# Kernel optimization log

Measured on AMD Instinct MI355X. Metric: run time of the kernel, lower is better.

## Reference

```python
import jax, jax.numpy as jnp
import numpy as np

TEMPERATURE = 0.07
EPS = 1e-12  # matches torch F.normalize default eps


def setup_inputs() -> dict:
    key = jax.random.key(0)
    k1, k2 = jax.random.split(key)
    features1 = jax.random.normal(k1, (16384, 512), dtype=jnp.float32)
    features2 = jax.random.normal(k2, (16384, 512), dtype=jnp.float32)
    return {"features1": features1, "features2": features2}


def _l2_normalize(x):
    # torch F.normalize: x / max(||x||, eps)
    norm = jnp.sqrt(jnp.sum(x * x, axis=1, keepdims=True))
    return x / jnp.maximum(norm, EPS)


def reference(features1, features2):
    f1 = _l2_normalize(features1)
    f2 = _l2_normalize(features2)
    # [N, N] similarity logits
    logits = jnp.einsum('nd,md->nm', f1, f2) / TEMPERATURE
    n = logits.shape[0]
    # cross-entropy with labels = arange(n): mean over rows of (logsumexp - diag logit)
    log_probs = jax.nn.log_softmax(logits, axis=1)
    diag = jnp.diagonal(log_probs)
    loss = -jnp.mean(diag)
    return loss
```

## Files before the change

### kernel.cpp

```cpp
#include <hip/hip_runtime.h>
#include <stdint.h>

#define NROWS 16384
#define KDIM  512
#define BM 128
#define BN 128
#define CT 4
#define NCHUNK 32
#define NPH 16
#define SLOT 16384
#define INV_T 14.285714285714286f
#define LOG2E 1.4426950408889634f

typedef __bf16 bf16x8 __attribute__((ext_vector_type(8)));
typedef float  f32x16 __attribute__((ext_vector_type(16)));
typedef unsigned short u16x8 __attribute__((ext_vector_type(8)));

__device__ __forceinline__ void gload_lds16(const void* gptr, void* lptr) {
    uint32_t loff = (uint32_t)(uintptr_t)lptr;
    loff = __builtin_amdgcn_readfirstlane(loff);
    __builtin_amdgcn_global_load_lds(
        (const uint32_t __attribute__((address_space(1)))*)(uintptr_t)gptr,
        (uint32_t __attribute__((address_space(3)))*)(uintptr_t)loff,
        16, 0, 0);
}


__global__ void k_norm(const float* __restrict__ X, char* __restrict__ Y, float scale) {
    const int row  = blockIdx.x * 4 + (threadIdx.x >> 6);
    const int lane = threadIdx.x & 63;
    const float* xr = X + (size_t)row * KDIM + lane * 8;
    float4 a = *(const float4*)xr;
    float4 b = *(const float4*)(xr + 4);
    float ss = a.x*a.x + a.y*a.y + a.z*a.z + a.w*a.w
             + b.x*b.x + b.y*b.y + b.z*b.z + b.w*b.w;
    #pragma unroll
    for (int off = 1; off < 64; off <<= 1) ss += __shfl_xor(ss, off);
    const float s = scale / fmaxf(sqrtf(ss), 1e-12f);
    __bf16 o[8];
    o[0] = (__bf16)(a.x * s); o[1] = (__bf16)(a.y * s);
    o[2] = (__bf16)(a.z * s); o[3] = (__bf16)(a.w * s);
    o[4] = (__bf16)(b.x * s); o[5] = (__bf16)(b.y * s);
    o[6] = (__bf16)(b.z * s); o[7] = (__bf16)(b.w * s);
    const int kh = lane >> 2, q = lane & 3;
    const size_t gr = ((size_t)(kh * 512 + (row >> 5)) * 2 + (q >> 1)) * 64
                    + ((q & 1) << 5) + (row & 31);
    *(u16x8*)(Y + gr * 16) = *(const u16x8*)o;
}

__global__ __launch_bounds__(256, 2) void k_gemm(const char* __restrict__ A,
                                                 const char* __restrict__ B,
                                                 float* __restrict__ S_part) {
    __shared__ __align__(16) char L[3 * SLOT];
    __shared__ float rowsum[2][BM];
    char* Lc = (char*)L;

    const int tid  = threadIdx.x;
    const int lane = tid & 63;
    const int w    = tid >> 6;
    const int wr   = w >> 1, wc = w & 1;
    const int bid  = blockIdx.x;
    const int xcd  = bid & 7;
    const int idx  = bid >> 3;
    const int st   = idx >> 5;
    const int wsub = idx & 31;
    const int sg   = xcd * 16 + st;
    const int bg   = sg & 15, cg = sg >> 4;
    const int brow  = (bg * 8 + (wsub >> 2)) * BM;
    const int chunk = cg * 4 + (wsub & 3);
    const int rbA0 = brow >> 5;

#define STGA(KH_, S_) do {                                                    \
        const char* g_ = A + ((size_t)((KH_) * 512 + rbA0) * 2048) + tid * 16;\
        char* l_ = Lc + (S_) * SLOT + tid * 16;                               \
        gload_lds16(g_,        l_);                                           \
        gload_lds16(g_ + 4096, l_ + 4096);                                    \
    } while (0)

#define STGB(KH_, S_) do {                                                    \
        const char* g_ = B + ((size_t)((KH_) * 512 + rbB0) * 2048) + tid * 16;\
        char* l_ = Lc + (S_) * SLOT + 8192 + tid * 16;                        \
        gload_lds16(g_,        l_);                                           \
        gload_lds16(g_ + 4096, l_ + 4096);                                    \
    } while (0)

#define RDS(HH_) do {                                                         \
        const char* sl_ = Lc + ((HH_) % 3) * SLOT;                            \
        _Pragma("unroll") for (int m_ = 0; m_ < 2; ++m_)                      \
        _Pragma("unroll") for (int ks_ = 0; ks_ < 2; ++ks_)                   \
            af[m_][ks_] = *(const bf16x8*)(sl_ + ((wr * 2 + m_) << 11)        \
                                           + (ks_ << 10) + (lane << 4));      \
        _Pragma("unroll") for (int n_ = 0; n_ < 2; ++n_)                      \
        _Pragma("unroll") for (int ks_ = 0; ks_ < 2; ++ks_)                   \
            bf[n_][ks_] = *(const bf16x8*)(sl_ + 8192 + ((wc * 2 + n_) << 11) \
                                           + (ks_ << 10) + (lane << 4));      \
    } while (0)

#define MM() do {                                                             \
        __builtin_amdgcn_s_setprio(1);                                        \
        _Pragma("unroll") for (int m_ = 0; m_ < 2; ++m_)                      \
        _Pragma("unroll") for (int n_ = 0; n_ < 2; ++n_)                      \
        _Pragma("unroll") for (int ks_ = 0; ks_ < 2; ++ks_)                   \
            acc[m_][n_] = __builtin_amdgcn_mfma_f32_32x32x16_bf16(            \
                af[m_][ks_], bf[n_][ks_], acc[m_][n_], 0, 0, 0);              \
        __builtin_amdgcn_s_setprio(0);                                        \
    } while (0)

    float rowacc = 0.f;
    #pragma unroll 1
    for (int ct = 0; ct < CT; ++ct) {
        const int rbB0 = chunk * 16 + ct * 4;
        f32x16 acc[2][2] = {};
        bf16x8 af[2][2], bf[2][2];

        STGA(0, 0); STGB(0, 0);
        STGA(1, 1); STGB(1, 1);
        asm volatile("s_waitcnt vmcnt(4)" ::: "memory");
        __builtin_amdgcn_s_barrier();

        #pragma unroll
        for (int h = 0; h < NPH; ++h) {
            RDS(h);
            if (h < NPH - 2) { STGA(h + 2, (h + 2) % 3); STGB(h + 2, (h + 2) % 3); }
            MM();
            if (h < NPH - 2)       asm volatile("s_waitcnt vmcnt(4)" ::: "memory");
            else if (h == NPH - 2) asm volatile("s_waitcnt vmcnt(0)" ::: "memory");
            __builtin_amdgcn_s_barrier();
        }

        #pragma unroll
        for (int m = 0; m < 2; ++m) {
            float rs[16];
            #pragma unroll
            for (int r = 0; r < 16; ++r)
                rs[r] = __builtin_amdgcn_exp2f(acc[m][0][r])
                      + __builtin_amdgcn_exp2f(acc[m][1][r]);
            #pragma unroll
            for (int off = 16; off >= 1; off >>= 1)
                #pragma unroll
                for (int r = 0; r < 16; ++r)
                    rs[r] += __shfl_xor(rs[r], off);
            if ((lane & 31) == 0) {
                const int rb = wr * 64 + m * 32 + (lane >> 5) * 4;
                #pragma unroll
                for (int r = 0; r < 16; ++r)
                    rowsum[wc][rb + (r & 3) + 8 * (r >> 2)] = rs[r];
            }
        }
        __syncthreads();
        if (tid < BM) rowacc += rowsum[0][tid] + rowsum[1][tid];
        __syncthreads();
    }
#undef STGA
#undef STGB
#undef RDS
#undef MM
    if (tid < BM) S_part[(size_t)chunk * NROWS + brow + tid] = rowacc;
}

__global__ void k_diag(const float* __restrict__ X1, const float* __restrict__ X2,
                       float* __restrict__ diag) {
    const int row  = blockIdx.x * 4 + (threadIdx.x >> 6);
    const int lane = threadIdx.x & 63;
    const float* x1 = X1 + (size_t)row * KDIM + lane * 8;
    const float* x2 = X2 + (size_t)row * KDIM + lane * 8;
    float4 a0 = *(const float4*)x1, a1 = *(const float4*)(x1 + 4);
    float4 b0 = *(const float4*)x2, b1 = *(const float4*)(x2 + 4);
    float s1 = a0.x*a0.x + a0.y*a0.y + a0.z*a0.z + a0.w*a0.w
             + a1.x*a1.x + a1.y*a1.y + a1.z*a1.z + a1.w*a1.w;
    float s2 = b0.x*b0.x + b0.y*b0.y + b0.z*b0.z + b0.w*b0.w
             + b1.x*b1.x + b1.y*b1.y + b1.z*b1.z + b1.w*b1.w;
    float dd = a0.x*b0.x + a0.y*b0.y + a0.z*b0.z + a0.w*b0.w
             + a1.x*b1.x + a1.y*b1.y + a1.z*b1.z + a1.w*b1.w;
    #pragma unroll
    for (int off = 1; off < 64; off <<= 1) {
        s1 += __shfl_xor(s1, off);
        s2 += __shfl_xor(s2, off);
        dd += __shfl_xor(dd, off);
    }
    if (lane == 0)
        diag[row] = dd / (fmaxf(sqrtf(s1), 1e-12f) * fmaxf(sqrtf(s2), 1e-12f)) * INV_T;
}

__global__ void k_loss(const float* __restrict__ S_part, const float* __restrict__ diag,
                       float* __restrict__ partial) {
    const int g = blockIdx.x * 256 + threadIdx.x;
    float S = 0.f;
    #pragma unroll
    for (int c = 0; c < NCHUNK; ++c) S += S_part[(size_t)c * NROWS + g];
    float v = logf(S) - diag[g];
    __shared__ float wsum[4];
    #pragma unroll
    for (int off = 1; off < 64; off <<= 1) v += __shfl_xor(v, off);
    if ((threadIdx.x & 63) == 0) wsum[threadIdx.x >> 6] = v;
    __syncthreads();
    if (threadIdx.x == 0) partial[blockIdx.x] = wsum[0] + wsum[1] + wsum[2] + wsum[3];
}

__global__ void k_final(const float* __restrict__ partial, float* __restrict__ out) {
    float v = partial[threadIdx.x];
    #pragma unroll
    for (int off = 1; off < 64; off <<= 1) v += __shfl_xor(v, off);
    if (threadIdx.x == 0) out[0] = v * (1.0f / (float)NROWS);
}

extern "C" void kernel_launch(void* const* d_in, const int* in_sizes, int n_in,
                              void* d_out, int out_size, void* d_ws, size_t ws_size,
                              hipStream_t stream) {
    const float* f1 = (const float*)d_in[0];
    const float* f2 = (const float*)d_in[1];
    float* out = (float*)d_out;

    char* ws = (char*)d_ws;
    char*  f1p   = ws;
    char*  f2p   = ws + (16u << 20);
    float* S_part = (float*)(ws + (32u << 20));
    float* diag   = (float*)(ws + (34u << 20));
    float* part   = (float*)(ws + (34u << 20) + (1u << 16));

    k_norm<<<dim3(NROWS / 4), dim3(256), 0, stream>>>(f1, f1p, INV_T * LOG2E);
    k_norm<<<dim3(NROWS / 4), dim3(256), 0, stream>>>(f2, f2p, 1.0f);
    k_gemm<<<dim3((NROWS / BM) * NCHUNK), dim3(256), 0, stream>>>(f1p, f2p, S_part);
    k_diag<<<dim3(NROWS / 4), dim3(256), 0, stream>>>(f1, f2, diag);
    k_loss<<<dim3(NROWS / 256), dim3(256), 0, stream>>>(S_part, diag, part);
    k_final<<<dim3(1), dim3(64), 0, stream>>>(part, out);
}
```

Measured before the change: 354.4 us.

## Use four-slot LDS ring and process two K-phases per barrier

The GEMM main loop moves from a three-slot LDS ring, with one K-phase and one barrier per step, to a four-slot ring. Each iteration now reads two K-phases into separate register fragment sets, stages the next two phases, and issues both sets of MFMAs before a single full vmcnt wait and barrier. The aim is to halve the barrier and waitcnt overhead and give the MFMAs larger batches. In exchange, shared memory per block grows to 64KB and fragment registers double. The full vmcnt(0) wait each iteration may also expose load latency that the old partial wait hid.

```diff
diff --git a/kernel.cpp b/kernel.cpp
--- a/kernel.cpp
+++ b/kernel.cpp
@@ -7,7 +7,7 @@
 #define BN 128
 #define CT 4
 #define NCHUNK 32
-#define NPH 16
+#define NIV 8
 #define SLOT 16384
 #define INV_T 14.285714285714286f
 #define LOG2E 1.4426950408889634f
@@ -51,7 +51,7 @@
 __global__ __launch_bounds__(256, 2) void k_gemm(const char* __restrict__ A,
                                                  const char* __restrict__ B,
                                                  float* __restrict__ S_part) {
-    __shared__ __align__(16) char L[3 * SLOT];
+    __shared__ __align__(16) char L[4 * SLOT];
     __shared__ float rowsum[2][BM];
     char* Lc = (char*)L;
 
@@ -84,25 +84,25 @@
         gload_lds16(g_ + 4096, l_ + 4096);                                    \
     } while (0)
 
-#define RDS(HH_) do {                                                         \
-        const char* sl_ = Lc + ((HH_) % 3) * SLOT;                            \
+#define RDS(SET_, HH_) do {                                                   \
+        const char* sl_ = Lc + ((HH_) & 3) * SLOT;                            \
         _Pragma("unroll") for (int m_ = 0; m_ < 2; ++m_)                      \
         _Pragma("unroll") for (int ks_ = 0; ks_ < 2; ++ks_)                   \
-            af[m_][ks_] = *(const bf16x8*)(sl_ + ((wr * 2 + m_) << 11)        \
+            af[SET_][m_][ks_] = *(const bf16x8*)(sl_ + ((wr * 2 + m_) << 11)  \
                                            + (ks_ << 10) + (lane << 4));      \
         _Pragma("unroll") for (int n_ = 0; n_ < 2; ++n_)                      \
         _Pragma("unroll") for (int ks_ = 0; ks_ < 2; ++ks_)                   \
-            bf[n_][ks_] = *(const bf16x8*)(sl_ + 8192 + ((wc * 2 + n_) << 11) \
-                                           + (ks_ << 10) + (lane << 4));      \
-    } while (0)
-
-#define MM() do {                                                             \
+            bf[SET_][n_][ks_] = *(const bf16x8*)(sl_ + 8192                   \
+                  + ((wc * 2 + n_) << 11) + (ks_ << 10) + (lane << 4));       \
+    } while (0)
+
+#define MM(SET_) do {                                                         \
         __builtin_amdgcn_s_setprio(1);                                        \
         _Pragma("unroll") for (int m_ = 0; m_ < 2; ++m_)                      \
         _Pragma("unroll") for (int n_ = 0; n_ < 2; ++n_)                      \
         _Pragma("unroll") for (int ks_ = 0; ks_ < 2; ++ks_)                   \
             acc[m_][n_] = __builtin_amdgcn_mfma_f32_32x32x16_bf16(            \
-                af[m_][ks_], bf[n_][ks_], acc[m_][n_], 0, 0, 0);              \
+                af[SET_][m_][ks_], bf[SET_][n_][ks_], acc[m_][n_], 0, 0, 0);  \
         __builtin_amdgcn_s_setprio(0);                                        \
     } while (0)
 
@@ -111,20 +111,26 @@
     for (int ct = 0; ct < CT; ++ct) {
         const int rbB0 = chunk * 16 + ct * 4;
         f32x16 acc[2][2] = {};
-        bf16x8 af[2][2], bf[2][2];
+        bf16x8 af[2][2][2], bf[2][2][2];
 
         STGA(0, 0); STGB(0, 0);
         STGA(1, 1); STGB(1, 1);
-        asm volatile("s_waitcnt vmcnt(4)" ::: "memory");
+        STGA(2, 2); STGB(2, 2);
+        STGA(3, 3); STGB(3, 3);
+        asm volatile("s_waitcnt vmcnt(8)" ::: "memory");
         __builtin_amdgcn_s_barrier();
 
         #pragma unroll
-        for (int h = 0; h < NPH; ++h) {
-            RDS(h);
-            if (h < NPH - 2) { STGA(h + 2, (h + 2) % 3); STGB(h + 2, (h + 2) % 3); }
-            MM();
-            if (h < NPH - 2)       asm volatile("s_waitcnt vmcnt(4)" ::: "memory");
-            else if (h == NPH - 2) asm volatile("s_waitcnt vmcnt(0)" ::: "memory");
+        for (int j = 0; j < NIV; ++j) {
+            RDS(0, 2 * j);
+            RDS(1, 2 * j + 1);
+            if (j >= 1 && j <= 6) {
+                STGA(2 * j + 2, (2 * j + 2) & 3); STGB(2 * j + 2, (2 * j + 2) & 3);
+                STGA(2 * j + 3, (2 * j + 3) & 3); STGB(2 * j + 3, (2 * j + 3) & 3);
+            }
+            MM(0);
+            MM(1);
+            asm volatile("s_waitcnt vmcnt(0)" ::: "memory");
             __builtin_amdgcn_s_barrier();
         }
 
```

After: 388.6 us. 9.6% more time.

## Load A fragments directly from global into double-buffered registers, stage only B via LDS

Applied to the files above, without the earlier changes.

The A operand of the similarity GEMM now bypasses shared memory. Each wave loads its A fragments straight from global memory into a register double buffer one k-phase ahead, and only B is staged through LDS with a three-slot ring. This halves LDS footprint and LDS read traffic and drops the explicit vmcnt waits inside the loop, relying instead on compiler-inserted waits for the register loads. In exchange, the two waves sharing A rows each fetch them from global or L2, which duplicates that traffic and raises register pressure. The correctness of the LDS staging now depends implicitly on in-order vmcnt completion.

```diff
diff --git a/kernel.cpp b/kernel.cpp
--- a/kernel.cpp
+++ b/kernel.cpp
@@ -8,7 +8,7 @@
 #define CT 4
 #define NCHUNK 32
 #define NPH 16
-#define SLOT 16384
+#define BSLOT 8192
 #define INV_T 14.285714285714286f
 #define LOG2E 1.4426950408889634f
 
@@ -51,7 +51,7 @@
 __global__ __launch_bounds__(256, 2) void k_gemm(const char* __restrict__ A,
                                                  const char* __restrict__ B,
                                                  float* __restrict__ S_part) {
-    __shared__ __align__(16) char L[3 * SLOT];
+    __shared__ __align__(16) char L[3 * BSLOT];
     __shared__ float rowsum[2][BM];
     char* Lc = (char*)L;
 
@@ -70,61 +70,63 @@
     const int chunk = cg * 4 + (wsub & 3);
     const int rbA0 = brow >> 5;
 
-#define STGA(KH_, S_) do {                                                    \
-        const char* g_ = A + ((size_t)((KH_) * 512 + rbA0) * 2048) + tid * 16;\
-        char* l_ = Lc + (S_) * SLOT + tid * 16;                               \
+#define LDA(S_, KH_) do {                                                     \
+        _Pragma("unroll") for (int m_ = 0; m_ < 2; ++m_)                      \
+        _Pragma("unroll") for (int ks_ = 0; ks_ < 2; ++ks_)                   \
+            aF[S_][m_][ks_] = *(const bf16x8*)(A                              \
+                + ((size_t)(((KH_) * 512 + rbA0 + wr * 2 + m_) * 2 + ks_) << 10) \
+                + (lane << 4));                                               \
+    } while (0)
+
+#define STGB(KH_, S_) do {                                                    \
+        const char* g_ = B + ((size_t)((KH_) * 512 + rbB0) * 2048) + tid * 16;\
+        char* l_ = Lc + (S_) * BSLOT + tid * 16;                              \
         gload_lds16(g_,        l_);                                           \
         gload_lds16(g_ + 4096, l_ + 4096);                                    \
     } while (0)
 
-#define STGB(KH_, S_) do {                                                    \
-        const char* g_ = B + ((size_t)((KH_) * 512 + rbB0) * 2048) + tid * 16;\
-        char* l_ = Lc + (S_) * SLOT + 8192 + tid * 16;                        \
-        gload_lds16(g_,        l_);                                           \
-        gload_lds16(g_ + 4096, l_ + 4096);                                    \
-    } while (0)
-
-#define RDS(HH_) do {                                                         \
-        const char* sl_ = Lc + ((HH_) % 3) * SLOT;                            \
-        _Pragma("unroll") for (int m_ = 0; m_ < 2; ++m_)                      \
-        _Pragma("unroll") for (int ks_ = 0; ks_ < 2; ++ks_)                   \
-            af[m_][ks_] = *(const bf16x8*)(sl_ + ((wr * 2 + m_) << 11)        \
-                                           + (ks_ << 10) + (lane << 4));      \
+#define RDSB(HH_) do {                                                        \
+        const char* sl_ = Lc + ((HH_) % 3) * BSLOT;                           \
         _Pragma("unroll") for (int n_ = 0; n_ < 2; ++n_)                      \
         _Pragma("unroll") for (int ks_ = 0; ks_ < 2; ++ks_)                   \
-            bf[n_][ks_] = *(const bf16x8*)(sl_ + 8192 + ((wc * 2 + n_) << 11) \
-                                           + (ks_ << 10) + (lane << 4));      \
-    } while (0)
-
-#define MM() do {                                                             \
+            bF[n_][ks_] = *(const bf16x8*)(sl_                                \
+                + (((wc * 2 + n_) * 2 + ks_) << 10) + (lane << 4));           \
+    } while (0)
+
+#define MM(SET_) do {                                                         \
         __builtin_amdgcn_s_setprio(1);                                        \
         _Pragma("unroll") for (int m_ = 0; m_ < 2; ++m_)                      \
         _Pragma("unroll") for (int n_ = 0; n_ < 2; ++n_)                      \
         _Pragma("unroll") for (int ks_ = 0; ks_ < 2; ++ks_)                   \
             acc[m_][n_] = __builtin_amdgcn_mfma_f32_32x32x16_bf16(            \
-                af[m_][ks_], bf[n_][ks_], acc[m_][n_], 0, 0, 0);              \
+                aF[SET_][m_][ks_], bF[n_][ks_], acc[m_][n_], 0, 0, 0);        \
         __builtin_amdgcn_s_setprio(0);                                        \
     } while (0)
 
     float rowacc = 0.f;
+    bf16x8 aF[2][2][2];
+    bf16x8 bF[2][2];
+
     #pragma unroll 1
     for (int ct = 0; ct < CT; ++ct) {
         const int rbB0 = chunk * 16 + ct * 4;
         f32x16 acc[2][2] = {};
-        bf16x8 af[2][2], bf[2][2];
-
-        STGA(0, 0); STGB(0, 0);
-        STGA(1, 1); STGB(1, 1);
-        asm volatile("s_waitcnt vmcnt(4)" ::: "memory");
+
+        STGB(0, 0);
+        STGB(1, 1);
+        __builtin_amdgcn_sched_barrier(0);
+        LDA(0, 0);
+        asm volatile("s_waitcnt vmcnt(0)" ::: "memory");
         __builtin_amdgcn_s_barrier();
 
         #pragma unroll
         for (int h = 0; h < NPH; ++h) {
-            RDS(h);
-            if (h < NPH - 2) { STGA(h + 2, (h + 2) % 3); STGB(h + 2, (h + 2) % 3); }
-            MM();
-            if (h < NPH - 2)       asm volatile("s_waitcnt vmcnt(4)" ::: "memory");
-            else if (h == NPH - 2) asm volatile("s_waitcnt vmcnt(0)" ::: "memory");
+            if (h < NPH - 2) STGB(h + 2, (h + 2) % 3);
+            __builtin_amdgcn_sched_barrier(0);
+            if (h < NPH - 1) LDA((h + 1) & 1, h + 1);
+            __builtin_amdgcn_sched_barrier(0);
+            RDSB(h);
+            MM(h & 1);
             __builtin_amdgcn_s_barrier();
         }
 
@@ -151,9 +153,9 @@
         if (tid < BM) rowacc += rowsum[0][tid] + rowsum[1][tid];
         __syncthreads();
     }
-#undef STGA
+#undef LDA
 #undef STGB
-#undef RDS
+#undef RDSB
 #undef MM
     if (tid < BM) S_part[(size_t)chunk * NROWS + brow + tid] = rowacc;
 }
```

New measurement: 606.9 us. 1.71x slower.
